# Kernel tuning notes

Measured on AMD Instinct MI355X. Metric: run time of the kernel, lower is better.

The kernel has to match this reference:

```python
import jax, jax.numpy as jnp
import numpy as np

B, C_IN, C_OUT = 4, 8, 8
P_IN, P_OUT = 16384, 4096
N_EVAL = 1_000_000
SPATIAL = 2
HID = 64
DECAY = (P_IN / 16) ** 2  # 1048576.0; bump support: ||z||^4 <= 1/DECAY -> ||z|| <= 1/32


def setup_inputs() -> dict:
    key = jax.random.key(0)
    ks = jax.random.split(key, 8)
    features = jax.random.normal(ks[0], (B, C_IN, P_IN), jnp.float32)
    # offsets inside the bump support (max ||z|| ~ 0.0283 < 0.03125 keeps 1 - DECAY*||z||^4 > 0)
    eval_locs = (jax.random.uniform(ks[1], (N_EVAL, SPATIAL), jnp.float32) * 2.0 - 1.0) * 0.02
    quad_weights = jax.random.uniform(ks[2], (P_IN,), jnp.float32, 0.5, 1.5) / P_IN
    # filter MLP: spatial_dim -> 64 -> 64 -> C_IN*C_OUT, Sin activations, no bias
    W0 = jax.random.normal(ks[3], (SPATIAL, HID), jnp.float32) / np.float32(np.sqrt(SPATIAL))
    W1 = jax.random.normal(ks[4], (HID, HID), jnp.float32) / np.float32(np.sqrt(HID))
    W2 = jax.random.normal(ks[5], (HID, C_IN * C_OUT), jnp.float32) / np.float32(np.sqrt(HID))
    eval_idx_out = jnp.sort(jax.random.randint(ks[6], (N_EVAL,), 0, P_OUT, jnp.int32))
    eval_idx_in = jax.random.randint(ks[7], (N_EVAL,), 0, P_IN, jnp.int32)
    return dict(features=features, eval_locs=eval_locs, quad_weights=quad_weights,
                W0=W0, W1=W1, W2=W2, eval_idx_out=eval_idx_out, eval_idx_in=eval_idx_in)


def reference(features, eval_locs, quad_weights, W0, W1, W2, eval_idx_out, eval_idx_in):
    # per-eval-point filter G(z): (N, C_in, C_out)
    h = jnp.sin(eval_locs @ W0)
    h = jnp.sin(h @ W1)
    filt = (h @ W2).reshape(-1, C_IN, C_OUT)
    # bump(z) = exp(1 - 1/(1 - decay*||z||^4))
    r4 = jnp.sum(eval_locs * eval_locs, axis=-1) ** 2          # (N,)
    bump = jnp.exp(1.0 - 1.0 / (1.0 - DECAY * r4))             # (N,)
    w = bump * quad_weights[eval_idx_in]                       # (N,)
    gathered = features[:, :, eval_idx_in]                     # (B, C_in, N)
    # fused bump/quad weighting + per-point matmul
    values = jnp.einsum('n,bin,nij->nbj', w, gathered, filt)   # (N, B, C_out)
    # scatter-reduce sum over output-point index
    integral = jax.ops.segment_sum(values, eval_idx_out, num_segments=P_OUT)  # (P_out, B, C_out)
    return jnp.transpose(integral, (1, 2, 0))                  # (B, C_out, P_out)
```

## Files before the change

### kernel.cpp

```cpp
#include <hip/hip_runtime.h>

#define NEV   1000000
#define POUT  4096
#define PIN   16384

typedef __bf16 bf16x8 __attribute__((ext_vector_type(8)));
typedef float  f32x16 __attribute__((ext_vector_type(16)));

#define SEG_OFF   0
#define FT_OFF    4160
#define FT_FLOATS (32 * PIN)

#define LH1_STRIDE 66
#define LWG_STRIDE 34
#define LH1_SIZE (32 * LH1_STRIDE)
#define LWG_SIZE (32 * LWG_STRIDE)

#define GEMM3(accv, ahi_, alo_, bhi_, blo_)                                          \
    accv = __builtin_amdgcn_mfma_f32_32x32x16_bf16(ahi_, bhi_, accv, 0, 0, 0);       \
    accv = __builtin_amdgcn_mfma_f32_32x32x16_bf16(ahi_, blo_, accv, 0, 0, 0);       \
    accv = __builtin_amdgcn_mfma_f32_32x32x16_bf16(alo_, bhi_, accv, 0, 0, 0);

__global__ __launch_bounds__(256) void prep_k(const float* __restrict__ f,
                                              const int* __restrict__ eio,
                                              float* __restrict__ ws) {
    const int bid = blockIdx.x, t = threadIdx.x;
    if (bid < 512) {
        __shared__ float tile[32][33];
        const int p0 = bid * 32;
        #pragma unroll
        for (int rep = 0; rep < 4; ++rep) {
            const int idx = rep * 256 + t;
            const int c = idx >> 5, pl = idx & 31;
            tile[pl][c] = f[c * PIN + p0 + pl];
        }
        __syncthreads();
        #pragma unroll
        for (int rep = 0; rep < 4; ++rep) {
            const int idx = rep * 256 + t;
            const int pl = idx >> 5, c = idx & 31;
            ws[FT_OFF + (p0 + pl) * 32 + c] = tile[pl][c];
        }
    } else {
        int* seg = (int*)ws + SEG_OFF;
        const int base = (bid - 512) * 1024 + t * 4;
        #pragma unroll
        for (int u = 0; u < 4; ++u) {
            const int e = base + u;
            if (e < NEV) {
                const int cur = eio[e];
                const int prev = (e == 0) ? -1 : eio[e - 1];
                for (int q = prev + 1; q <= cur; ++q) seg[q] = e;
                if (e == NEV - 1) { for (int q = cur + 1; q <= POUT; ++q) seg[q] = NEV; }
            }
        }
    }
}

template <int MODE>
__global__ __launch_bounds__(256, 2) void quadconv_mfma_k(
    const float* __restrict__ features,
    const float* __restrict__ eval_locs,
    const float* __restrict__ quad_weights,
    const float* __restrict__ W0,
    const float* __restrict__ W1,
    const float* __restrict__ W2,
    const int* __restrict__ eio,
    const int* __restrict__ eii,
    const float* __restrict__ ws,
    float* __restrict__ out)
{
    __shared__ unsigned int lh1[4][LH1_SIZE];
    __shared__ unsigned int lwg[4][LWG_SIZE];
    const int tid  = threadIdx.x;
    const int wid  = tid >> 6;
    const int lane = tid & 63;
    const int n    = lane & 31;
    const int hl   = lane >> 5;
    const int p    = blockIdx.x * 4 + wid;

    int start, end;
    if constexpr (MODE == 0) {
        const int* seg = (const int*)ws + SEG_OFF;
        start = seg[p]; end = seg[p + 1];
    } else {
        int lo = 0, hi = NEV;
        while (lo < hi) { int m = (lo + hi) >> 1; if (eio[m] < p) lo = m + 1; else hi = m; }
        start = lo; hi = NEV;
        while (lo < hi) { int m = (lo + hi) >> 1; if (eio[m] <= p) lo = m + 1; else hi = m; }
        end = lo;
    }

    bf16x8 a1hi[2][4], a1lo[2][4];
    #pragma unroll
    for (int mb = 0; mb < 2; ++mb) {
        #pragma unroll
        for (int t = 0; t < 4; ++t) {
            #pragma unroll
            for (int e = 0; e < 8; ++e) {
                const int k = 8 * hl + e + 16 * t;
                const float v1 = W1[k * 64 + n + 32 * mb];
                const __bf16 h1b = (__bf16)v1;
                a1hi[mb][t][e] = h1b;
                a1lo[mb][t][e] = (__bf16)(v1 - (float)h1b);
            }
        }
    }

    f32x16 T[2];
    #pragma unroll
    for (int mb = 0; mb < 2; ++mb)
        #pragma unroll
        for (int r = 0; r < 16; ++r) T[mb][r] = 0.f;

    unsigned int* Lh = lh1[wid];
    unsigned int* Lw = lwg[wid];
    const int nt = (end - start + 31) >> 5;

    for (int tile = 0; tile < nt; ++tile) {
        const int e  = start + tile * 32 + n;
        const bool valid = (e < end);
        const int ec = valid ? e : (end - 1);
        const float2 x = ((const float2*)eval_locs)[ec];
        const int ii = eii[ec];

        const float r2 = x.x * x.x + x.y * x.y;
        const float dd = 1.0f - 1048576.0f * r2 * r2;
        float wgt = __expf(1.0f - 1.0f / dd) * quad_weights[ii];
        if (!valid) wgt = 0.f;

        f32x16 acc1[2];
        #pragma unroll
        for (int mb = 0; mb < 2; ++mb)
            #pragma unroll
            for (int r = 0; r < 16; ++r) acc1[mb][r] = 0.f;

        #pragma unroll
        for (int t = 0; t < 4; ++t) {
            const int k0 = 16 * t + 8 * hl;
            const float4 wa0 = *(const float4*)(W0 + k0);
            const float4 wa1 = *(const float4*)(W0 + k0 + 4);
            const float4 wb0 = *(const float4*)(W0 + 64 + k0);
            const float4 wb1 = *(const float4*)(W0 + 64 + k0 + 4);
            bf16x8 bhi, blo;
            {
                float s;  __bf16 hb;
                s = __sinf(fmaf(x.x, wa0.x, x.y * wb0.x)); hb = (__bf16)s; bhi[0] = hb; blo[0] = (__bf16)(s - (float)hb);
                s = __sinf(fmaf(x.x, wa0.y, x.y * wb0.y)); hb = (__bf16)s; bhi[1] = hb; blo[1] = (__bf16)(s - (float)hb);
                s = __sinf(fmaf(x.x, wa0.z, x.y * wb0.z)); hb = (__bf16)s; bhi[2] = hb; blo[2] = (__bf16)(s - (float)hb);
                s = __sinf(fmaf(x.x, wa0.w, x.y * wb0.w)); hb = (__bf16)s; bhi[3] = hb; blo[3] = (__bf16)(s - (float)hb);
                s = __sinf(fmaf(x.x, wa1.x, x.y * wb1.x)); hb = (__bf16)s; bhi[4] = hb; blo[4] = (__bf16)(s - (float)hb);
                s = __sinf(fmaf(x.x, wa1.y, x.y * wb1.y)); hb = (__bf16)s; bhi[5] = hb; blo[5] = (__bf16)(s - (float)hb);
                s = __sinf(fmaf(x.x, wa1.z, x.y * wb1.z)); hb = (__bf16)s; bhi[6] = hb; blo[6] = (__bf16)(s - (float)hb);
                s = __sinf(fmaf(x.x, wa1.w, x.y * wb1.w)); hb = (__bf16)s; bhi[7] = hb; blo[7] = (__bf16)(s - (float)hb);
            }
            #pragma unroll
            for (int mb = 0; mb < 2; ++mb) { GEMM3(acc1[mb], a1hi[mb][t], a1lo[mb][t], bhi, blo); }
        }

        #pragma unroll
        for (int mb = 0; mb < 2; ++mb) {
            #pragma unroll
            for (int rq = 0; rq < 4; ++rq) {
                const int j0 = 8 * rq + 4 * hl + 32 * mb;
                unsigned int u[4];
                #pragma unroll
                for (int s4 = 0; s4 < 4; ++s4) {
                    const float s = __sinf(acc1[mb][4 * rq + s4]);
                    const __bf16 hb = (__bf16)s;
                    const __bf16 lb = (__bf16)(s - (float)hb);
                    u[s4] = ((unsigned int)__builtin_bit_cast(unsigned short, hb) << 16) |
                             (unsigned int)__builtin_bit_cast(unsigned short, lb);
                }
                *(uint2*)&Lh[n * LH1_STRIDE + j0]     = make_uint2(u[0], u[1]);
                *(uint2*)&Lh[n * LH1_STRIDE + j0 + 2] = make_uint2(u[2], u[3]);
            }
        }

        {
            float g[16];
            if constexpr (MODE == 0) {
                const float4* gp = (const float4*)(ws + FT_OFF + ii * 32 + 16 * hl);
                const float4 G0 = gp[0], G1 = gp[1], G2 = gp[2], G3 = gp[3];
                g[0]=G0.x; g[1]=G0.y; g[2]=G0.z; g[3]=G0.w;
                g[4]=G1.x; g[5]=G1.y; g[6]=G1.z; g[7]=G1.w;
                g[8]=G2.x; g[9]=G2.y; g[10]=G2.z; g[11]=G2.w;
                g[12]=G3.x; g[13]=G3.y; g[14]=G3.z; g[15]=G3.w;
            } else {
                #pragma unroll
                for (int v = 0; v < 16; ++v) g[v] = features[(16 * hl + v) * PIN + ii];
            }
            #pragma unroll
            for (int v2 = 0; v2 < 8; ++v2) {
                unsigned int u[2];
                #pragma unroll
                for (int s4 = 0; s4 < 2; ++s4) {
                    const float wv = wgt * g[2 * v2 + s4];
                    const __bf16 hb = (__bf16)wv;
                    const __bf16 lb = (__bf16)(wv - (float)hb);
                    u[s4] = ((unsigned int)__builtin_bit_cast(unsigned short, hb) << 16) |
                             (unsigned int)__builtin_bit_cast(unsigned short, lb);
                }
                *(uint2*)&Lw[n * LWG_STRIDE + 16 * hl + 2 * v2] = make_uint2(u[0], u[1]);
            }
        }

        #pragma unroll
        for (int kt = 0; kt < 2; ++kt) {
            bf16x8 bh, bl;
            #pragma unroll
            for (int q = 0; q < 8; ++q) {
                const unsigned int u = Lw[(16 * kt + 8 * hl + q) * LWG_STRIDE + n];
                bh[q] = __builtin_bit_cast(__bf16, (unsigned short)(u >> 16));
                bl[q] = __builtin_bit_cast(__bf16, (unsigned short)(u & 0xffffu));
            }
            #pragma unroll
            for (int mb = 0; mb < 2; ++mb) {
                bf16x8 ah, al;
                #pragma unroll
                for (int q = 0; q < 8; ++q) {
                    const unsigned int u = Lh[(16 * kt + 8 * hl + q) * LH1_STRIDE + n + 32 * mb];
                    ah[q] = __builtin_bit_cast(__bf16, (unsigned short)(u >> 16));
                    al[q] = __builtin_bit_cast(__bf16, (unsigned short)(u & 0xffffu));
                }
                GEMM3(T[mb], ah, al, bh, bl);
            }
        }
    }

    {
        const int i = n & 7, b = n >> 3;
        float pj[8];
        #pragma unroll
        for (int j = 0; j < 8; ++j) pj[j] = 0.f;
        #pragma unroll
        for (int mb = 0; mb < 2; ++mb) {
            #pragma unroll
            for (int r = 0; r < 16; ++r) {
                const int khid = (r & 3) + 8 * (r >> 2) + 4 * hl + 32 * mb;
                const float tv = T[mb][r];
                const float4 w20 = *(const float4*)(W2 + khid * 64 + i * 8);
                const float4 w21 = *(const float4*)(W2 + khid * 64 + i * 8 + 4);
                pj[0] = fmaf(tv, w20.x, pj[0]);
                pj[1] = fmaf(tv, w20.y, pj[1]);
                pj[2] = fmaf(tv, w20.z, pj[2]);
                pj[3] = fmaf(tv, w20.w, pj[3]);
                pj[4] = fmaf(tv, w21.x, pj[4]);
                pj[5] = fmaf(tv, w21.y, pj[5]);
                pj[6] = fmaf(tv, w21.z, pj[6]);
                pj[7] = fmaf(tv, w21.w, pj[7]);
            }
        }
        #pragma unroll
        for (int j = 0; j < 8; ++j) {
            float v = pj[j];
            v += __shfl_xor(v, 1);
            v += __shfl_xor(v, 2);
            v += __shfl_xor(v, 4);
            v += __shfl_xor(v, 32);
            pj[j] = v;
        }
        if (i == 0 && hl == 0) {
            #pragma unroll
            for (int j = 0; j < 8; ++j) out[b * (8 * POUT) + j * POUT + p] = pj[j];
        }
    }
}

extern "C" void kernel_launch(void* const* d_in, const int* in_sizes, int n_in,
                              void* d_out, int out_size, void* d_ws, size_t ws_size,
                              hipStream_t stream) {
    const float* features  = (const float*)d_in[0];
    const float* eval_locs = (const float*)d_in[1];
    const float* qw        = (const float*)d_in[2];
    const float* W0        = (const float*)d_in[3];
    const float* W1        = (const float*)d_in[4];
    const float* W2        = (const float*)d_in[5];
    const int*   eio       = (const int*)d_in[6];
    const int*   eii       = (const int*)d_in[7];
    float* out = (float*)d_out;
    float* ws  = (float*)d_ws;

    const size_t need0 = (size_t)(FT_OFF + FT_FLOATS) * 4;
    if (ws_size >= need0) {
        prep_k<<<512 + (NEV + 1023) / 1024, 256, 0, stream>>>(features, eio, ws);
        quadconv_mfma_k<0><<<POUT / 4, 256, 0, stream>>>(features, eval_locs, qw, W0, W1, W2,
                                                         eio, eii, ws, out);
    } else {
        quadconv_mfma_k<2><<<POUT / 4, 256, 0, stream>>>(features, eval_locs, qw, W0, W1, W2,
                                                         eio, eii, ws, out);
    }
}
```

Measured before the change: 152.3 us.

## Transpose LDS staging layout, pack hi/lo bf16 with perm, binary-search segment offsets

Reworks the shared-memory staging of the hidden activations and weighted features into a transposed layout. Readers can now fetch packed hi/lo pairs with 128-bit LDS loads and split them with byte-perm instructions, instead of issuing eight scalar loads plus shifts per operand. The hi/lo bf16 split is computed by bit masking and a single perm rather than by conversions. The segment-start prep now runs one binary search per output point over a few blocks, replacing per-eval-point fill loops across about a thousand blocks. This cuts launch work but adds dependent global loads per search.

```diff
diff --git a/kernel.cpp b/kernel.cpp
--- a/kernel.cpp
+++ b/kernel.cpp
@@ -11,10 +11,18 @@
 #define FT_OFF    4160
 #define FT_FLOATS (32 * PIN)
 
-#define LH1_STRIDE 66
-#define LWG_STRIDE 34
-#define LH1_SIZE (32 * LH1_STRIDE)
-#define LWG_SIZE (32 * LWG_STRIDE)
+#define LH_ST 36
+#define LW_ST 36
+
+#define SEL_HI 0x07060302u
+#define SEL_LO 0x05040100u
+
+__device__ __forceinline__ unsigned pack_hl(float v) {
+    const unsigned b = __builtin_bit_cast(unsigned, v);
+    const float hb = __builtin_bit_cast(float, b & 0xFFFF0000u);
+    const float lo = v - hb;
+    return __builtin_amdgcn_perm(b, __builtin_bit_cast(unsigned, lo), SEL_HI);
+}
 
 #define GEMM3(accv, ahi_, alo_, bhi_, blo_)                                          \
     accv = __builtin_amdgcn_mfma_f32_32x32x16_bf16(ahi_, bhi_, accv, 0, 0, 0);       \
@@ -43,17 +51,11 @@
         }
     } else {
         int* seg = (int*)ws + SEG_OFF;
-        const int base = (bid - 512) * 1024 + t * 4;
-        #pragma unroll
-        for (int u = 0; u < 4; ++u) {
-            const int e = base + u;
-            if (e < NEV) {
-                const int cur = eio[e];
-                const int prev = (e == 0) ? -1 : eio[e - 1];
-                for (int q = prev + 1; q <= cur; ++q) seg[q] = e;
-                if (e == NEV - 1) { for (int q = cur + 1; q <= POUT; ++q) seg[q] = NEV; }
-            }
-        }
+        const int q = (bid - 512) * 256 + t;
+        int lo = 0, hi = NEV;
+        while (lo < hi) { int m = (lo + hi) >> 1; if (eio[m] < q) lo = m + 1; else hi = m; }
+        seg[q] = lo;
+        if (q == 0) seg[POUT] = NEV;
     }
 }
 
@@ -70,8 +72,8 @@
     const float* __restrict__ ws,
     float* __restrict__ out)
 {
-    __shared__ unsigned int lh1[4][LH1_SIZE];
-    __shared__ unsigned int lwg[4][LWG_SIZE];
+    __shared__ unsigned lh[4][64 * LH_ST];
+    __shared__ unsigned lw[4][32 * LW_ST];
     const int tid  = threadIdx.x;
     const int wid  = tid >> 6;
     const int lane = tid & 63;
@@ -96,14 +98,21 @@
     for (int mb = 0; mb < 2; ++mb) {
         #pragma unroll
         for (int t = 0; t < 4; ++t) {
-            #pragma unroll
-            for (int e = 0; e < 8; ++e) {
-                const int k = 8 * hl + e + 16 * t;
-                const float v1 = W1[k * 64 + n + 32 * mb];
-                const __bf16 h1b = (__bf16)v1;
-                a1hi[mb][t][e] = h1b;
-                a1lo[mb][t][e] = (__bf16)(v1 - (float)h1b);
-            }
+            unsigned hw[4], lw_[4];
+            #pragma unroll
+            for (int i = 0; i < 4; ++i) {
+                const float v0 = W1[(8 * hl + 2 * i + 16 * t) * 64 + n + 32 * mb];
+                const float v1 = W1[(8 * hl + 2 * i + 1 + 16 * t) * 64 + n + 32 * mb];
+                const unsigned b0 = __builtin_bit_cast(unsigned, v0);
+                const unsigned b1 = __builtin_bit_cast(unsigned, v1);
+                const float l0 = v0 - __builtin_bit_cast(float, b0 & 0xFFFF0000u);
+                const float l1 = v1 - __builtin_bit_cast(float, b1 & 0xFFFF0000u);
+                hw[i]  = __builtin_amdgcn_perm(b1, b0, SEL_HI);
+                lw_[i] = __builtin_amdgcn_perm(__builtin_bit_cast(unsigned, l1),
+                                               __builtin_bit_cast(unsigned, l0), SEL_HI);
+            }
+            a1hi[mb][t] = __builtin_bit_cast(bf16x8, make_uint4(hw[0], hw[1], hw[2], hw[3]));
+            a1lo[mb][t] = __builtin_bit_cast(bf16x8, make_uint4(lw_[0], lw_[1], lw_[2], lw_[3]));
         }
     }
 
@@ -113,8 +122,11 @@
         #pragma unroll
         for (int r = 0; r < 16; ++r) T[mb][r] = 0.f;
 
-    unsigned int* Lh = lh1[wid];
-    unsigned int* Lw = lwg[wid];
+    unsigned* Lhw = &lh[wid][4 * hl * LH_ST + n];
+    unsigned* Lww = &lw[wid][16 * hl * LW_ST + n];
+    const unsigned* Lhr = &lh[wid][n * LH_ST + 8 * hl];
+    const unsigned* Lwr = &lw[wid][n * LW_ST + 8 * hl];
+
     const int nt = (end - start + 31) >> 5;
 
     for (int tile = 0; tile < nt; ++tile) {
@@ -138,42 +150,33 @@
         #pragma unroll
         for (int t = 0; t < 4; ++t) {
             const int k0 = 16 * t + 8 * hl;
-            const float4 wa0 = *(const float4*)(W0 + k0);
-            const float4 wa1 = *(const float4*)(W0 + k0 + 4);
-            const float4 wb0 = *(const float4*)(W0 + 64 + k0);
-            const float4 wb1 = *(const float4*)(W0 + 64 + k0 + 4);
-            bf16x8 bhi, blo;
-            {
-                float s;  __bf16 hb;
-                s = __sinf(fmaf(x.x, wa0.x, x.y * wb0.x)); hb = (__bf16)s; bhi[0] = hb; blo[0] = (__bf16)(s - (float)hb);
-                s = __sinf(fmaf(x.x, wa0.y, x.y * wb0.y)); hb = (__bf16)s; bhi[1] = hb; blo[1] = (__bf16)(s - (float)hb);
-                s = __sinf(fmaf(x.x, wa0.z, x.y * wb0.z)); hb = (__bf16)s; bhi[2] = hb; blo[2] = (__bf16)(s - (float)hb);
-                s = __sinf(fmaf(x.x, wa0.w, x.y * wb0.w)); hb = (__bf16)s; bhi[3] = hb; blo[3] = (__bf16)(s - (float)hb);
-                s = __sinf(fmaf(x.x, wa1.x, x.y * wb1.x)); hb = (__bf16)s; bhi[4] = hb; blo[4] = (__bf16)(s - (float)hb);
-                s = __sinf(fmaf(x.x, wa1.y, x.y * wb1.y)); hb = (__bf16)s; bhi[5] = hb; blo[5] = (__bf16)(s - (float)hb);
-                s = __sinf(fmaf(x.x, wa1.z, x.y * wb1.z)); hb = (__bf16)s; bhi[6] = hb; blo[6] = (__bf16)(s - (float)hb);
-                s = __sinf(fmaf(x.x, wa1.w, x.y * wb1.w)); hb = (__bf16)s; bhi[7] = hb; blo[7] = (__bf16)(s - (float)hb);
-            }
-            #pragma unroll
-            for (int mb = 0; mb < 2; ++mb) { GEMM3(acc1[mb], a1hi[mb][t], a1lo[mb][t], bhi, blo); }
+            float s[8];
+            #pragma unroll
+            for (int q = 0; q < 8; ++q)
+                s[q] = __sinf(fmaf(x.x, W0[k0 + q], x.y * W0[64 + k0 + q]));
+            unsigned hw[4], lw_[4];
+            #pragma unroll
+            for (int i = 0; i < 4; ++i) {
+                const unsigned b0 = __builtin_bit_cast(unsigned, s[2 * i]);
+                const unsigned b1 = __builtin_bit_cast(unsigned, s[2 * i + 1]);
+                const float l0 = s[2 * i]     - __builtin_bit_cast(float, b0 & 0xFFFF0000u);
+                const float l1 = s[2 * i + 1] - __builtin_bit_cast(float, b1 & 0xFFFF0000u);
+                hw[i]  = __builtin_amdgcn_perm(b1, b0, SEL_HI);
+                lw_[i] = __builtin_amdgcn_perm(__builtin_bit_cast(unsigned, l1),
+                                               __builtin_bit_cast(unsigned, l0), SEL_HI);
+            }
+            const bf16x8 bhi = __builtin_bit_cast(bf16x8, make_uint4(hw[0], hw[1], hw[2], hw[3]));
+            const bf16x8 blo = __builtin_bit_cast(bf16x8, make_uint4(lw_[0], lw_[1], lw_[2], lw_[3]));
+            GEMM3(acc1[0], a1hi[0][t], a1lo[0][t], bhi, blo);
+            GEMM3(acc1[1], a1hi[1][t], a1lo[1][t], bhi, blo);
         }
 
         #pragma unroll
         for (int mb = 0; mb < 2; ++mb) {
             #pragma unroll
-            for (int rq = 0; rq < 4; ++rq) {
-                const int j0 = 8 * rq + 4 * hl + 32 * mb;
-                unsigned int u[4];
-                #pragma unroll
-                for (int s4 = 0; s4 < 4; ++s4) {
-                    const float s = __sinf(acc1[mb][4 * rq + s4]);
-                    const __bf16 hb = (__bf16)s;
-                    const __bf16 lb = (__bf16)(s - (float)hb);
-                    u[s4] = ((unsigned int)__builtin_bit_cast(unsigned short, hb) << 16) |
-                             (unsigned int)__builtin_bit_cast(unsigned short, lb);
-                }
-                *(uint2*)&Lh[n * LH1_STRIDE + j0]     = make_uint2(u[0], u[1]);
-                *(uint2*)&Lh[n * LH1_STRIDE + j0 + 2] = make_uint2(u[2], u[3]);
+            for (int r = 0; r < 16; ++r) {
+                const int row = ((r & 3) + 8 * (r >> 2) + 32 * mb);
+                Lhw[row * LH_ST] = pack_hl(__sinf(acc1[mb][r]));
             }
         }
 
@@ -191,38 +194,37 @@
                 for (int v = 0; v < 16; ++v) g[v] = features[(16 * hl + v) * PIN + ii];
             }
             #pragma unroll
-            for (int v2 = 0; v2 < 8; ++v2) {
-                unsigned int u[2];
-                #pragma unroll
-                for (int s4 = 0; s4 < 2; ++s4) {
-                    const float wv = wgt * g[2 * v2 + s4];
-                    const __bf16 hb = (__bf16)wv;
-                    const __bf16 lb = (__bf16)(wv - (float)hb);
-                    u[s4] = ((unsigned int)__builtin_bit_cast(unsigned short, hb) << 16) |
-                             (unsigned int)__builtin_bit_cast(unsigned short, lb);
-                }
-                *(uint2*)&Lw[n * LWG_STRIDE + 16 * hl + 2 * v2] = make_uint2(u[0], u[1]);
-            }
+            for (int v = 0; v < 16; ++v) Lww[v * LW_ST] = pack_hl(wgt * g[v]);
         }
 
         #pragma unroll
         for (int kt = 0; kt < 2; ++kt) {
-            bf16x8 bh, bl;
-            #pragma unroll
-            for (int q = 0; q < 8; ++q) {
-                const unsigned int u = Lw[(16 * kt + 8 * hl + q) * LWG_STRIDE + n];
-                bh[q] = __builtin_bit_cast(__bf16, (unsigned short)(u >> 16));
-                bl[q] = __builtin_bit_cast(__bf16, (unsigned short)(u & 0xffffu));
-            }
+            const uint4 p0 = *(const uint4*)(Lwr + 16 * kt);
+            const uint4 p1 = *(const uint4*)(Lwr + 16 * kt + 4);
+            const bf16x8 bh = __builtin_bit_cast(bf16x8, make_uint4(
+                __builtin_amdgcn_perm(p0.y, p0.x, SEL_HI),
+                __builtin_amdgcn_perm(p0.w, p0.z, SEL_HI),
+                __builtin_amdgcn_perm(p1.y, p1.x, SEL_HI),
+                __builtin_amdgcn_perm(p1.w, p1.z, SEL_HI)));
+            const bf16x8 bl = __builtin_bit_cast(bf16x8, make_uint4(
+                __builtin_amdgcn_perm(p0.y, p0.x, SEL_LO),
+                __builtin_amdgcn_perm(p0.w, p0.z, SEL_LO),
+                __builtin_amdgcn_perm(p1.y, p1.x, SEL_LO),
+                __builtin_amdgcn_perm(p1.w, p1.z, SEL_LO)));
             #pragma unroll
             for (int mb = 0; mb < 2; ++mb) {
-                bf16x8 ah, al;
-                #pragma unroll
-                for (int q = 0; q < 8; ++q) {
-                    const unsigned int u = Lh[(16 * kt + 8 * hl + q) * LH1_STRIDE + n + 32 * mb];
-                    ah[q] = __builtin_bit_cast(__bf16, (unsigned short)(u >> 16));
-                    al[q] = __builtin_bit_cast(__bf16, (unsigned short)(u & 0xffffu));
-                }
+                const uint4 q0 = *(const uint4*)(Lhr + 32 * mb * LH_ST + 16 * kt);
+                const uint4 q1 = *(const uint4*)(Lhr + 32 * mb * LH_ST + 16 * kt + 4);
+                const bf16x8 ah = __builtin_bit_cast(bf16x8, make_uint4(
+                    __builtin_amdgcn_perm(q0.y, q0.x, SEL_HI),
+                    __builtin_amdgcn_perm(q0.w, q0.z, SEL_HI),
+                    __builtin_amdgcn_perm(q1.y, q1.x, SEL_HI),
+                    __builtin_amdgcn_perm(q1.w, q1.z, SEL_HI)));
+                const bf16x8 al = __builtin_bit_cast(bf16x8, make_uint4(
+                    __builtin_amdgcn_perm(q0.y, q0.x, SEL_LO),
+                    __builtin_amdgcn_perm(q0.w, q0.z, SEL_LO),
+                    __builtin_amdgcn_perm(q1.y, q1.x, SEL_LO),
+                    __builtin_amdgcn_perm(q1.w, q1.z, SEL_LO)));
                 GEMM3(T[mb], ah, al, bh, bl);
             }
         }
@@ -283,7 +285,7 @@
 
     const size_t need0 = (size_t)(FT_OFF + FT_FLOATS) * 4;
     if (ws_size >= need0) {
-        prep_k<<<512 + (NEV + 1023) / 1024, 256, 0, stream>>>(features, eio, ws);
+        prep_k<<<512 + POUT / 256, 256, 0, stream>>>(features, eio, ws);
         quadconv_mfma_k<0><<<POUT / 4, 256, 0, stream>>>(features, eval_locs, qw, W0, W1, W2,
                                                          eio, eii, ws, out);
     } else {
```

New measurement: 140.2 us. -8.0%, faster.
